# Optimization experiments

Measured on AMD Instinct MI355X. Metric: run time of the kernel, lower is better.

The kernel has to match this reference:

```python
import jax, jax.numpy as jnp
import numpy as np

N_NEIGHBORS = 9
MIN_STD, MAX_STD = 0.01, 0.5
EPS_NORM = 1e-8


def setup_inputs() -> dict:
    key = jax.random.key(0)
    k1, k2, k3 = jax.random.split(key, 3)
    B, C, H, W = 8, 1024, 28, 28
    M, D = 16384, 1024
    features = jax.random.normal(k1, (B, C, H, W), dtype=jnp.float32)
    memory_bank = jax.random.normal(k2, (M, D), dtype=jnp.float32)
    influence_weight = jnp.ones((D,), dtype=jnp.float32)
    distance_weight = jnp.ones((1,), dtype=jnp.float32)
    eps = jax.random.normal(k3, (B * H * W, D), dtype=jnp.float32)  # randn_like noise
    return {"features": features, "memory_bank": memory_bank,
            "influence_weight": influence_weight, "distance_weight": distance_weight,
            "eps": eps}


def reference(features, memory_bank, influence_weight, distance_weight, eps):
    B, C, H, W = features.shape
    M, D = memory_bank.shape
    x = features.transpose(0, 2, 3, 1).reshape(B * H * W, C)  # [N, D]
    N = x.shape[0]

    d2 = (jnp.sum(x * x, axis=1, keepdims=True)
          + jnp.sum(memory_bank * memory_bank, axis=1)[None, :]
          - 2.0 * (x @ memory_bank.T))  # [N, M]
    dist = jnp.sqrt(jnp.clip(d2, 1e-12))

    k = min(N_NEIGHBORS, M)
    neg_topd, idx = jax.lax.top_k(-dist, k)  # smallest-k distances
    topk_distances = -neg_topd  # [N, k]

    # Per-dimension influence: mean |x - nn| over k neighbors, scaled by weight
    nn_feats = memory_bank[idx]  # [N, k, D] gather
    influence = jnp.abs(x[:, None, :] - nn_feats).mean(axis=1) * influence_weight[None, :]  # [N, D]

    # Row-wise normalization (torch std is unbiased, ddof=1)
    infl_norm = ((influence - influence.mean(axis=-1, keepdims=True))
                 / (jnp.std(influence, axis=-1, ddof=1, keepdims=True) + EPS_NORM))

    # Distance signal: per-row mean distance, normalized by global stats of the
    # [N, D]-expanded tensor (each row value repeated D times -> same mean,
    # unbiased std uses N*D - 1 in the denominator).
    ds = topk_distances.mean(axis=-1, keepdims=True)  # [N, 1]
    full_mean = ds.mean()
    full_std = jnp.sqrt(jnp.sum((ds - full_mean) ** 2) * D / (N * D - 1))
    dist_norm = (ds - full_mean) / (full_std + EPS_NORM)  # [N, 1], broadcasts over D

    combined = infl_norm + distance_weight * dist_norm  # [N, D]
    noise_std = MIN_STD + (MAX_STD - MIN_STD) * jax.nn.sigmoid(combined)

    noised = (x + eps * noise_std).reshape(B, H, W, C).transpose(0, 3, 1, 2)
    influence_map = influence.mean(axis=-1).reshape(B, H, W)
    noise_std_map = noise_std.mean(axis=-1).reshape(B, H, W)
    return noised, influence_map, noise_std_map
```

## Files before the change

### kernel.cpp

```cpp
#include <hip/hip_runtime.h>
#include <hip/hip_bf16.h>
#include <stdint.h>

#define N_ROWS 6272
#define DIM    1024
#define M_ROWS 16384
#define KNN    9
#define BMS    128
#define BNS    128
#define NPANEL 128
#define TOPC   6
#define NCAND  (NPANEL * 2 * TOPC)
#define TRR    16
#define LSTR   160

typedef __attribute__((ext_vector_type(4))) float f32x4;
typedef __attribute__((ext_vector_type(4))) int   i32x4;
typedef __attribute__((ext_vector_type(16))) int  i32x16;

#define QSCALE 31.75f

__device__ __forceinline__ int quant8(float v) {
  return __float2int_rn(fminf(fmaxf(v, -4.f), 4.f) * QSCALE);
}

__device__ __forceinline__ int kswz(int row, int col) {
  return col ^ ((row & 7) << 2) ^ (((row >> 3) & 1) << 5);
}

__global__ void k_prep_x(const float* __restrict__ feat,
                         float* __restrict__ xf, signed char* __restrict__ xq) {
  __shared__ float tile[32][33];
  const int ct = blockIdx.x & 31, nt = blockIdx.x >> 5;
  const int c0 = ct * 32, n0 = nt * 32;
  const int tx = threadIdx.x & 31, ty = threadIdx.x >> 5;
  {
    const int n = n0 + tx;
    const int b = n / 784, hw = n % 784;
    const float* src = feat + (size_t)b * 802816 + hw;
#pragma unroll
    for (int q = 0; q < 4; ++q)
      tile[ty + q * 8][tx] = src[(size_t)(c0 + ty + q * 8) * 784];
  }
  __syncthreads();
#pragma unroll
  for (int q = 0; q < 4; ++q) {
    const int nn = n0 + ty + q * 8;
    const int cc = c0 + tx;
    const float v = tile[tx][ty + q * 8];
    xf[(size_t)nn * DIM + cc] = v;
    xq[(size_t)nn * DIM + cc] = (signed char)quant8(v);
  }
}

__global__ void k_prep_m(const float* __restrict__ mb,
                         signed char* __restrict__ mq, int* __restrict__ mni) {
  const int j = blockIdx.x;
  const int t = threadIdx.x;
  const float* src = mb + (size_t)j * DIM;
  signed char* dst = mq + (size_t)j * DIM;
  int s = 0;
  for (int c = t; c < DIM; c += 256) {
    const int q = quant8(src[c]);
    dst[c] = (signed char)q;
    s += q * q;
  }
  __shared__ int red[4];
#pragma unroll
  for (int o = 32; o >= 1; o >>= 1) s += __shfl_down(s, o);
  if ((t & 63) == 0) red[t >> 6] = s;
  __syncthreads();
  if (t == 0) mni[j] = red[0] + red[1] + red[2] + red[3];
}

__launch_bounds__(256, 2)
__global__ void k_score(const signed char* __restrict__ xq,
                        const signed char* __restrict__ mq,
                        const int* __restrict__ mni,
                        unsigned int* __restrict__ cand) {
  __shared__ signed char S[81920];
  int* Kbuf = (int*)S;

  const int bx = blockIdx.x;
  const int xcd = bx & 7, i = bx >> 3;
  const int panel = i & 15, agroup = i >> 4;
  const int j0 = xcd * 2048 + panel * BNS;
  const int pglob = xcd * 16 + panel;

  const int t = threadIdx.x;
  const int lane = t & 63, w = t >> 6;
  const int wr = w >> 1, wc = w & 1;
  const int l31 = lane & 31, kh = lane >> 5;

  int srcOff[4], ldsOff[4];
#pragma unroll
  for (int cpy = 0; cpy < 4; ++cpy) {
    const int c = cpy * 256 + t;
    const int row = c >> 3, s = c & 7;
    srcOff[cpy] = row * DIM + s * 16;
    ldsOff[cpy] = row * LSTR + ((s ^ (row & 7)) << 4);
  }
  const signed char* bBase = mq + (size_t)j0 * DIM;

  int mn_[2];
#pragma unroll
  for (int ni = 0; ni < 2; ++ni) mn_[ni] = mni[j0 + wc * 64 + ni * 32 + l31];

  const int tcount = (agroup == 0) ? 13 : 12;
#pragma unroll 1
  for (int k7 = 0; k7 < tcount; ++k7) {
    const int tile = agroup + 4 * k7;
    const int r0 = tile * BMS;
    const signed char* aBase = xq + (size_t)r0 * DIM;

    i32x16 acc[2][2];
#pragma unroll
    for (int mi = 0; mi < 2; ++mi)
#pragma unroll
      for (int ni = 0; ni < 2; ++ni)
#pragma unroll
        for (int r = 0; r < 16; ++r) acc[mi][ni][r] = 0;

    i32x4 ra[4], rb[4];
#pragma unroll
    for (int cpy = 0; cpy < 4; ++cpy) {
      ra[cpy] = *(const i32x4*)(aBase + srcOff[cpy]);
      rb[cpy] = *(const i32x4*)(bBase + srcOff[cpy]);
    }
#pragma unroll
    for (int cpy = 0; cpy < 4; ++cpy) {
      *(i32x4*)(S + ldsOff[cpy]) = ra[cpy];
      *(i32x4*)(S + 40960 + ldsOff[cpy]) = rb[cpy];
    }
    asm volatile("s_waitcnt lgkmcnt(0)" ::: "memory");
    __builtin_amdgcn_s_barrier();

#pragma unroll 1
    for (int kt = 0; kt < 8; ++kt) {
      const int cb = (kt & 1) * 20480;
      const signed char* Ab = S + cb;
      const signed char* Bb = S + 40960 + cb;
      if (kt < 7) {
        const int kk = (kt + 1) * 128;
#pragma unroll
        for (int cpy = 0; cpy < 4; ++cpy) {
          ra[cpy] = *(const i32x4*)(aBase + srcOff[cpy] + kk);
          rb[cpy] = *(const i32x4*)(bBase + srcOff[cpy] + kk);
        }
      }
      __builtin_amdgcn_s_setprio(1);
#pragma unroll
      for (int ks = 0; ks < 4; ++ks) {
        const int sr = 2 * ks + kh;
        i32x4 a[2], b[2];
#pragma unroll
        for (int mi = 0; mi < 2; ++mi) {
          const int r = wr * 64 + mi * 32 + l31;
          a[mi] = *(const i32x4*)(Ab + r * LSTR + ((sr ^ (r & 7)) << 4));
        }
#pragma unroll
        for (int ni = 0; ni < 2; ++ni) {
          const int r = wc * 64 + ni * 32 + l31;
          b[ni] = *(const i32x4*)(Bb + r * LSTR + ((sr ^ (r & 7)) << 4));
        }
#pragma unroll
        for (int mi = 0; mi < 2; ++mi)
#pragma unroll
          for (int ni = 0; ni < 2; ++ni)
            acc[mi][ni] = __builtin_amdgcn_mfma_i32_32x32x32_i8(a[mi], b[ni], acc[mi][ni], 0, 0, 0);
      }
      __builtin_amdgcn_s_setprio(0);
      if (kt < 7) {
        const int nb = ((kt + 1) & 1) * 20480;
#pragma unroll
        for (int cpy = 0; cpy < 4; ++cpy) {
          *(i32x4*)(S + nb + ldsOff[cpy]) = ra[cpy];
          *(i32x4*)(S + 40960 + nb + ldsOff[cpy]) = rb[cpy];
        }
      }
      asm volatile("s_waitcnt lgkmcnt(0)" ::: "memory");
      __builtin_amdgcn_s_barrier();
    }

#pragma unroll
    for (int mi = 0; mi < 2; ++mi)
#pragma unroll
      for (int ni = 0; ni < 2; ++ni) {
        const int col = wc * 64 + ni * 32 + l31;
        const int mn = mn_[ni];
#pragma unroll
        for (int r = 0; r < 16; ++r) {
          const int row = wr * 64 + mi * 32 + 4 * kh + (r & 3) + 8 * (r >> 2);
          Kbuf[row * 128 + kswz(row, col)] = mn - 2 * acc[mi][ni][r];
        }
      }
    __syncthreads();
    {
      const int row = t >> 1, half = t & 1;
      unsigned tk[TOPC];
#pragma unroll
      for (int s = 0; s < TOPC; ++s) tk[s] = 0xFFFFFFFFu;
#pragma unroll
      for (int q = 0; q < 16; ++q) {
        const int cl = half * 64 + q * 4;
        const i32x4 v = *(const i32x4*)(Kbuf + row * 128 + kswz(row, cl));
#pragma unroll
        for (int e = 0; e < 4; ++e) {
          const unsigned p = (((unsigned)(v[e] + (1 << 25)) >> 11) << 14)
                             | (unsigned)(j0 + cl + e);
          if (p < tk[0]) {
            tk[0] = p;
#pragma unroll
            for (int s = 0; s < TOPC - 1; ++s) {
              const unsigned hi = tk[s] > tk[s + 1] ? tk[s] : tk[s + 1];
              const unsigned lo = tk[s] > tk[s + 1] ? tk[s + 1] : tk[s];
              tk[s] = hi; tk[s + 1] = lo;
            }
          }
        }
      }
      const size_t base = (size_t)(r0 + row) * NCAND + (size_t)(pglob * 2 + half) * TOPC;
#pragma unroll
      for (int s = 0; s < TOPC; ++s) cand[base + s] = tk[s];
    }
    __syncthreads();
  }
}

__global__ void k_rerank(const float* __restrict__ xf, const float* __restrict__ mb,
                         const unsigned int* __restrict__ cand,
                         int* __restrict__ idx9, double* __restrict__ dsv) {
  const int n = blockIdx.x, t = threadIdx.x;
  __shared__ float    xs[DIM];
  __shared__ unsigned cs[NCAND];
  __shared__ unsigned sel[TRR];
  __shared__ double dpart[256];
  __shared__ double d2s[TRR];
  __shared__ double dist_s[TRR];
  __shared__ int    rank_s[TRR];

  const float* xrow = xf + (size_t)n * DIM;
  for (int c = t; c < DIM; c += 256) xs[c] = xrow[c];
  const size_t cb = (size_t)n * NCAND;
  for (int s = t; s < NCAND; s += 256) cs[s] = cand[cb + s];
  __syncthreads();

  if (t < 64) {
    unsigned ck[24];
#pragma unroll
    for (int s = 0; s < 24; ++s) ck[s] = cs[t + 64 * s];
    for (int it = 0; it < TRR; ++it) {
      unsigned best = ck[0];
#pragma unroll
      for (int s = 1; s < 24; ++s) best = best < ck[s] ? best : ck[s];
#pragma unroll
      for (int off = 32; off >= 1; off >>= 1) {
        const unsigned o = (unsigned)__shfl_xor((int)best, off);
        best = best < o ? best : o;
      }
      if (t == 0) sel[it] = best;
#pragma unroll
      for (int s = 0; s < 24; ++s) if (ck[s] == best) ck[s] = 0xFFFFFFFFu;
    }
  }
  __syncthreads();
  {
    const int s = t >> 4, l16 = t & 15;
    const int j = (int)(sel[s] & 16383u);
    const float* mrow = mb + (size_t)j * DIM;
    double a = 0.0;
    for (int i = 0; i < 64; ++i) {
      const int c = l16 + (i << 4);
      const double d = (double)xs[c] - (double)mrow[c];
      a += d * d;
    }
    dpart[t] = a;
  }
  __syncthreads();
  if (t < TRR) {
    double v = 0.0;
    for (int i = 0; i < 16; ++i) v += dpart[t * 16 + i];
    d2s[t] = v;
    dist_s[t] = sqrt(v < 1e-12 ? 1e-12 : v);
  }
  __syncthreads();
  if (t < TRR) {
    const double v = d2s[t]; const int id = (int)(sel[t] & 16383u);
    int r = 0;
    for (int u = 0; u < TRR; ++u) {
      const double vu = d2s[u];
      const int idu = (int)(sel[u] & 16383u);
      if (vu < v || (vu == v && idu < id)) ++r;
    }
    rank_s[t] = r;
    if (r < KNN) idx9[n * KNN + r] = id;
  }
  __syncthreads();
  if (t == 0) {
    double sum = 0.0;
    for (int u = 0; u < TRR; ++u) if (rank_s[u] < KNN) sum += dist_s[u];
    dsv[n] = sum * (1.0 / KNN);
  }
}

__global__ void k_dsstats(const double* __restrict__ dsv, double* __restrict__ stats) {
  __shared__ double red[1024];
  const int t = threadIdx.x;
  double s = 0.0;
  for (int i = t; i < N_ROWS; i += 1024) s += dsv[i];
  red[t] = s; __syncthreads();
  for (int o = 512; o >= 1; o >>= 1) { if (t < o) red[t] += red[t + o]; __syncthreads(); }
  const double mean = red[0] / (double)N_ROWS;
  __syncthreads();
  double v = 0.0;
  for (int i = t; i < N_ROWS; i += 1024) { const double d = dsv[i] - mean; v += d * d; }
  red[t] = v; __syncthreads();
  for (int o = 512; o >= 1; o >>= 1) { if (t < o) red[t] += red[t + o]; __syncthreads(); }
  if (t == 0) {
    const double fullstd = sqrt(red[0] * (double)DIM / ((double)N_ROWS * DIM - 1.0));
    stats[0] = mean;
    stats[1] = fullstd + 1e-8;
  }
}

__global__ void k_final(const float* __restrict__ xf, const float* __restrict__ mb,
                        const float* __restrict__ iw, const float* __restrict__ dwp,
                        const float* __restrict__ eps, const int* __restrict__ idx9,
                        const double* __restrict__ dsv, const double* __restrict__ stats,
                        float* __restrict__ out) {
  const int n = blockIdx.x, t = threadIdx.x;
  __shared__ float xs[DIM];
  __shared__ int js[KNN];
  __shared__ float rs1[4], rs2[4];
  const float* xrow = xf + (size_t)n * DIM;
  for (int c = t; c < DIM; c += 256) xs[c] = xrow[c];
  if (t < KNN) js[t] = idx9[n * KNN + t];
  __syncthreads();

  float infl[4];
  float s1 = 0.f, s2 = 0.f;
#pragma unroll
  for (int q = 0; q < 4; ++q) {
    const int c = t + q * 256;
    const float x = xs[c];
    float a = 0.f;
#pragma unroll
    for (int k = 0; k < KNN; ++k) a += fabsf(x - mb[(size_t)js[k] * DIM + c]);
    const float v = a * (1.0f / KNN) * iw[c];
    infl[q] = v; s1 += v; s2 += v * v;
  }
#pragma unroll
  for (int o = 32; o >= 1; o >>= 1) { s1 += __shfl_down(s1, o); s2 += __shfl_down(s2, o); }
  if ((t & 63) == 0) { rs1[t >> 6] = s1; rs2[t >> 6] = s2; }
  __syncthreads();
  const float sum = rs1[0] + rs1[1] + rs1[2] + rs1[3];
  const float sq  = rs2[0] + rs2[1] + rs2[2] + rs2[3];
  const float mean = sum * (1.0f / DIM);
  float var = (sq - (float)DIM * mean * mean) * (1.0f / (DIM - 1));
  var = fmaxf(var, 0.f);
  const float inv = 1.0f / (sqrtf(var) + 1e-8f);
  const float dn = (float)(((double)dsv[n] - stats[0]) / stats[1]);
  const float zb = dwp[0] * dn;

  const int b = n / 784, hw = n % 784;
  float* op = out + (size_t)b * (1024 * 784) + hw;
  const float* ep = eps + (size_t)n * DIM;
  float si = 0.f, sn = 0.f;
#pragma unroll
  for (int q = 0; q < 4; ++q) {
    const int c = t + q * 256;
    const float v = infl[q];
    const float z = (v - mean) * inv + zb;
    const float ns = 0.01f + 0.49f / (1.0f + expf(-z));
    op[(size_t)c * 784] = xs[c] + ep[c] * ns;
    si += v; sn += ns;
  }
  __syncthreads();
#pragma unroll
  for (int o = 32; o >= 1; o >>= 1) { si += __shfl_down(si, o); sn += __shfl_down(sn, o); }
  if ((t & 63) == 0) { rs1[t >> 6] = si; rs2[t >> 6] = sn; }
  __syncthreads();
  if (t == 0) {
    out[6422528 + n]        = (rs1[0] + rs1[1] + rs1[2] + rs1[3]) * (1.0f / DIM);
    out[6422528 + 6272 + n] = (rs2[0] + rs2[1] + rs2[2] + rs2[3]) * (1.0f / DIM);
  }
}

extern "C" void kernel_launch(void* const* d_in, const int* in_sizes, int n_in,
                              void* d_out, int out_size, void* d_ws, size_t ws_size,
                              hipStream_t stream) {
  (void)in_sizes; (void)n_in; (void)out_size; (void)ws_size;
  const float* feat = (const float*)d_in[0];
  const float* mb   = (const float*)d_in[1];
  const float* iw   = (const float*)d_in[2];
  const float* dw   = (const float*)d_in[3];
  const float* eps  = (const float*)d_in[4];
  float* out = (float*)d_out;

  char* p = (char*)d_ws;
  float* xf = (float*)p;                     p += (size_t)N_ROWS * DIM * 4;
  signed char* xq = (signed char*)p;         p += (size_t)N_ROWS * DIM;
  signed char* mq = (signed char*)p;         p += (size_t)M_ROWS * DIM;
  int* mni = (int*)p;                        p += (size_t)M_ROWS * 4;
  unsigned int* cand = (unsigned int*)p;     p += (size_t)N_ROWS * NCAND * 4;
  int* idx9 = (int*)p;                       p += (size_t)N_ROWS * KNN * 4;
  p = (char*)(((uintptr_t)p + 255) & ~(uintptr_t)255);
  double* dsv = (double*)p;                  p += (size_t)N_ROWS * 8;
  double* stats = (double*)p;                p += 64;

  k_prep_x<<<N_ROWS, 256, 0, stream>>>(feat, xf, xq);
  k_prep_m<<<M_ROWS, 256, 0, stream>>>(mb, mq, mni);
  k_score<<<512, 256, 0, stream>>>(xq, mq, mni, cand);
  k_rerank<<<N_ROWS, 256, 0, stream>>>(xf, mb, cand, idx9, dsv);
  k_dsstats<<<1, 1024, 0, stream>>>(dsv, stats);
  k_final<<<N_ROWS, 256, 0, stream>>>(xf, mb, iw, dw, eps, idx9, dsv, stats, out);
}
```

Measured before the change: 386.5 us.

## Halve k_score LDS footprint to run four blocks per CU with more blocks

The scoring GEMM drops LDS double-buffering and shrinks the top-k staging buffer to 64 columns at a time. This cuts shared memory from 80 KB to 40 KB so launch bounds can target four blocks per CU. The grid doubles to 1024 blocks, each covering fewer row tiles. The per-row top-6 is now built from two 32-column partial lists per 64-column half, merged by rank counting. The trade is extra barriers with no load/compute overlap inside a block, and a tighter register budget that may cause spills of the 64 accumulator registers.

```diff
diff --git a/kernel.cpp b/kernel.cpp
--- a/kernel.cpp
+++ b/kernel.cpp
@@ -24,10 +24,6 @@
   return __float2int_rn(fminf(fmaxf(v, -4.f), 4.f) * QSCALE);
 }
 
-__device__ __forceinline__ int kswz(int row, int col) {
-  return col ^ ((row & 7) << 2) ^ (((row >> 3) & 1) << 5);
-}
-
 __global__ void k_prep_x(const float* __restrict__ feat,
                          float* __restrict__ xf, signed char* __restrict__ xq) {
   __shared__ float tile[32][33];
@@ -73,13 +69,14 @@
   if (t == 0) mni[j] = red[0] + red[1] + red[2] + red[3];
 }
 
-__launch_bounds__(256, 2)
+__launch_bounds__(256, 4)
 __global__ void k_score(const signed char* __restrict__ xq,
                         const signed char* __restrict__ mq,
                         const int* __restrict__ mni,
                         unsigned int* __restrict__ cand) {
-  __shared__ signed char S[81920];
+  __shared__ signed char S[40960];
   int* Kbuf = (int*)S;
+  unsigned* stage6 = (unsigned*)(S + 32768);
 
   const int bx = blockIdx.x;
   const int xcd = bx & 7, i = bx >> 3;
@@ -106,10 +103,10 @@
 #pragma unroll
   for (int ni = 0; ni < 2; ++ni) mn_[ni] = mni[j0 + wc * 64 + ni * 32 + l31];
 
-  const int tcount = (agroup == 0) ? 13 : 12;
+  const int tcount = (agroup == 0) ? 7 : 6;
 #pragma unroll 1
   for (int k7 = 0; k7 < tcount; ++k7) {
-    const int tile = agroup + 4 * k7;
+    const int tile = agroup + 8 * k7;
     const int r0 = tile * BMS;
     const signed char* aBase = xq + (size_t)r0 * DIM;
 
@@ -127,19 +124,16 @@
       ra[cpy] = *(const i32x4*)(aBase + srcOff[cpy]);
       rb[cpy] = *(const i32x4*)(bBase + srcOff[cpy]);
     }
-#pragma unroll
-    for (int cpy = 0; cpy < 4; ++cpy) {
-      *(i32x4*)(S + ldsOff[cpy]) = ra[cpy];
-      *(i32x4*)(S + 40960 + ldsOff[cpy]) = rb[cpy];
-    }
-    asm volatile("s_waitcnt lgkmcnt(0)" ::: "memory");
-    __builtin_amdgcn_s_barrier();
 
 #pragma unroll 1
     for (int kt = 0; kt < 8; ++kt) {
-      const int cb = (kt & 1) * 20480;
-      const signed char* Ab = S + cb;
-      const signed char* Bb = S + 40960 + cb;
+      __syncthreads();
+#pragma unroll
+      for (int cpy = 0; cpy < 4; ++cpy) {
+        *(i32x4*)(S + ldsOff[cpy]) = ra[cpy];
+        *(i32x4*)(S + 20480 + ldsOff[cpy]) = rb[cpy];
+      }
+      __syncthreads();
       if (kt < 7) {
         const int kk = (kt + 1) * 128;
 #pragma unroll
@@ -156,12 +150,12 @@
 #pragma unroll
         for (int mi = 0; mi < 2; ++mi) {
           const int r = wr * 64 + mi * 32 + l31;
-          a[mi] = *(const i32x4*)(Ab + r * LSTR + ((sr ^ (r & 7)) << 4));
+          a[mi] = *(const i32x4*)(S + r * LSTR + ((sr ^ (r & 7)) << 4));
         }
 #pragma unroll
         for (int ni = 0; ni < 2; ++ni) {
           const int r = wc * 64 + ni * 32 + l31;
-          b[ni] = *(const i32x4*)(Bb + r * LSTR + ((sr ^ (r & 7)) << 4));
+          b[ni] = *(const i32x4*)(S + 20480 + r * LSTR + ((sr ^ (r & 7)) << 4));
         }
 #pragma unroll
         for (int mi = 0; mi < 2; ++mi)
@@ -170,58 +164,70 @@
             acc[mi][ni] = __builtin_amdgcn_mfma_i32_32x32x32_i8(a[mi], b[ni], acc[mi][ni], 0, 0, 0);
       }
       __builtin_amdgcn_s_setprio(0);
-      if (kt < 7) {
-        const int nb = ((kt + 1) & 1) * 20480;
-#pragma unroll
-        for (int cpy = 0; cpy < 4; ++cpy) {
-          *(i32x4*)(S + nb + ldsOff[cpy]) = ra[cpy];
-          *(i32x4*)(S + 40960 + nb + ldsOff[cpy]) = rb[cpy];
-        }
-      }
-      asm volatile("s_waitcnt lgkmcnt(0)" ::: "memory");
-      __builtin_amdgcn_s_barrier();
-    }
-
-#pragma unroll
-    for (int mi = 0; mi < 2; ++mi)
-#pragma unroll
-      for (int ni = 0; ni < 2; ++ni) {
-        const int col = wc * 64 + ni * 32 + l31;
-        const int mn = mn_[ni];
-#pragma unroll
-        for (int r = 0; r < 16; ++r) {
-          const int row = wr * 64 + mi * 32 + 4 * kh + (r & 3) + 8 * (r >> 2);
-          Kbuf[row * 128 + kswz(row, col)] = mn - 2 * acc[mi][ni][r];
-        }
-      }
-    __syncthreads();
-    {
-      const int row = t >> 1, half = t & 1;
-      unsigned tk[TOPC];
-#pragma unroll
-      for (int s = 0; s < TOPC; ++s) tk[s] = 0xFFFFFFFFu;
-#pragma unroll
-      for (int q = 0; q < 16; ++q) {
-        const int cl = half * 64 + q * 4;
-        const i32x4 v = *(const i32x4*)(Kbuf + row * 128 + kswz(row, cl));
-#pragma unroll
-        for (int e = 0; e < 4; ++e) {
-          const unsigned p = (((unsigned)(v[e] + (1 << 25)) >> 11) << 14)
-                             | (unsigned)(j0 + cl + e);
-          if (p < tk[0]) {
-            tk[0] = p;
-#pragma unroll
-            for (int s = 0; s < TOPC - 1; ++s) {
-              const unsigned hi = tk[s] > tk[s + 1] ? tk[s] : tk[s + 1];
-              const unsigned lo = tk[s] > tk[s + 1] ? tk[s + 1] : tk[s];
-              tk[s] = hi; tk[s + 1] = lo;
+    }
+
+#pragma unroll 1
+    for (int st = 0; st < 2; ++st) {
+      __syncthreads();
+      if (wc == st) {
+#pragma unroll
+        for (int mi = 0; mi < 2; ++mi)
+#pragma unroll
+          for (int ni = 0; ni < 2; ++ni) {
+            const int col = ni * 32 + l31;
+            const int mn = mn_[ni];
+#pragma unroll
+            for (int r = 0; r < 16; ++r) {
+              const int row = wr * 64 + mi * 32 + 4 * kh + (r & 3) + 8 * (r >> 2);
+              Kbuf[row * 64 + (col ^ ((row & 15) << 2))] = mn - 2 * acc[mi][ni][r];
+            }
+          }
+      }
+      __syncthreads();
+      {
+        const int row = t & 127, sub = t >> 7;
+        unsigned tk[TOPC];
+#pragma unroll
+        for (int s = 0; s < TOPC; ++s) tk[s] = 0xFFFFFFFFu;
+#pragma unroll
+        for (int q = 0; q < 8; ++q) {
+          const int cl = sub * 32 + q * 4;
+          const i32x4 v = *(const i32x4*)(Kbuf + row * 64 + (cl ^ ((row & 15) << 2)));
+#pragma unroll
+          for (int e = 0; e < 4; ++e) {
+            const unsigned p = (((unsigned)(v[e] + (1 << 25)) >> 11) << 14)
+                               | (unsigned)(j0 + st * 64 + cl + e);
+            if (p < tk[0]) {
+              tk[0] = p;
+#pragma unroll
+              for (int s = 0; s < TOPC - 1; ++s) {
+                const unsigned hi = tk[s] > tk[s + 1] ? tk[s] : tk[s + 1];
+                const unsigned lo = tk[s] > tk[s + 1] ? tk[s + 1] : tk[s];
+                tk[s] = hi; tk[s + 1] = lo;
+              }
             }
           }
         }
-      }
-      const size_t base = (size_t)(r0 + row) * NCAND + (size_t)(pglob * 2 + half) * TOPC;
-#pragma unroll
-      for (int s = 0; s < TOPC; ++s) cand[base + s] = tk[s];
+#pragma unroll
+        for (int s = 0; s < TOPC; ++s) stage6[t * TOPC + s] = tk[s];
+      }
+      __syncthreads();
+      if (t < 128) {
+        const size_t base = (size_t)(r0 + t) * NCAND + (size_t)(pglob * 2 + st) * TOPC;
+#pragma unroll
+        for (int i2 = 0; i2 < TOPC; ++i2) {
+          const unsigned va = stage6[t * TOPC + i2];
+          int ca = (TOPC - 1) - i2;
+#pragma unroll
+          for (int j2 = 0; j2 < TOPC; ++j2) ca += (stage6[(t + 128) * TOPC + j2] < va);
+          if (ca < TOPC) cand[base + ca] = va;
+          const unsigned vb = stage6[(t + 128) * TOPC + i2];
+          int cb = (TOPC - 1) - i2;
+#pragma unroll
+          for (int j2 = 0; j2 < TOPC; ++j2) cb += (stage6[t * TOPC + j2] < vb);
+          if (cb < TOPC) cand[base + cb] = vb;
+        }
+      }
     }
     __syncthreads();
   }
@@ -408,9 +414,9 @@
   double* dsv = (double*)p;                  p += (size_t)N_ROWS * 8;
   double* stats = (double*)p;                p += 64;
 
-  k_prep_x<<<N_ROWS, 256, 0, stream>>>(feat, xf, xq);
+  k_prep_x<<<6272, 256, 0, stream>>>(feat, xf, xq);
   k_prep_m<<<M_ROWS, 256, 0, stream>>>(mb, mq, mni);
-  k_score<<<512, 256, 0, stream>>>(xq, mq, mni, cand);
+  k_score<<<1024, 256, 0, stream>>>(xq, mq, mni, cand);
   k_rerank<<<N_ROWS, 256, 0, stream>>>(xf, mb, cand, idx9, dsv);
   k_dsstats<<<1, 1024, 0, stream>>>(dsv, stats);
   k_final<<<N_ROWS, 256, 0, stream>>>(xf, mb, iw, dw, eps, idx9, dsv, stats, out);
```

Measured after the change: 622.4 us. +61.0%, slower.
